# Kernel tuning notes

Measured on AMD Instinct MI355X. Metric: run time of the kernel, lower is better.

## Reference

```python
import jax, jax.numpy as jnp
import numpy as np

B, C, H, W, HEADS = 4, 192, 128, 128, 8
C2 = 2 * C
DN = ('NCHW', 'OIHW', 'NCHW')


def conv1x1(x, w, b):
    o = jax.lax.conv_general_dilated(x, w, (1, 1), 'VALID', dimension_numbers=DN)
    return o + b[None, :, None, None]


def gconv3(x, w, b):
    # grouped 3x3 conv: groups = C, channels = 2C -> 2 in / 2 out channels per group
    o = jax.lax.conv_general_dilated(x, w, (1, 1), 'SAME', dimension_numbers=DN,
                                     feature_group_count=C)
    return o + b[None, :, None, None]


def l2norm(t):
    # torch F.normalize(dim=-1, eps=1e-12)
    n = jnp.linalg.norm(t, axis=-1, keepdims=True)
    return t / jnp.maximum(n, 1e-12)


def setup_inputs() -> dict:
    key = jax.random.key(0)
    ks = jax.random.split(key, 16)
    s = 0.02
    inp = {
        'x': jax.random.normal(ks[0], (B, C, H, W), jnp.float32),
        'y': jax.random.normal(ks[1], (B, C, H, W), jnp.float32),
        'kv_w': jax.random.normal(ks[2], (C2, C, 1, 1), jnp.float32) * s,
        'kv_b': jax.random.normal(ks[3], (C2,), jnp.float32) * s,
        'kv_dw_w': jax.random.normal(ks[4], (C2, 2, 3, 3), jnp.float32) * s,
        'kv_dw_b': jax.random.normal(ks[5], (C2,), jnp.float32) * s,
        'q_w': jax.random.normal(ks[6], (C2, C, 1, 1), jnp.float32) * s,
        'q_b': jax.random.normal(ks[7], (C2,), jnp.float32) * s,
        'q_dw_w': jax.random.normal(ks[8], (C2, 2, 3, 3), jnp.float32) * s,
        'q_dw_b': jax.random.normal(ks[9], (C2,), jnp.float32) * s,
        'ky_w': jax.random.normal(ks[10], (C2, C, 1, 1), jnp.float32) * s,
        'ky_b': jax.random.normal(ks[11], (C2,), jnp.float32) * s,
        'ky_dw_w': jax.random.normal(ks[12], (C2, 2, 3, 3), jnp.float32) * s,
        'ky_dw_b': jax.random.normal(ks[13], (C2,), jnp.float32) * s,
        'temperature': jnp.ones((HEADS, 1, 1), jnp.float32),
        'gamma1': jnp.full((1,), 0.1, jnp.float32),
        'gamma2': jnp.full((1,), 0.1, jnp.float32),
    }
    return inp


def reference(x, y, kv_w, kv_b, kv_dw_w, kv_dw_b, q_w, q_b, q_dw_w, q_dw_b,
              ky_w, ky_b, ky_dw_w, ky_dw_b, temperature, gamma1, gamma2):
    b, c, h, w = x.shape
    ch = c // HEADS  # channels per head

    x_mid = x + y
    q = gconv3(conv1x1(x_mid, kv_w, kv_b), kv_dw_w, kv_dw_b)
    q1, q2 = jnp.split(q, 2, axis=1)
    kvx = gconv3(conv1x1(x, q_w, q_b), q_dw_w, q_dw_b)
    kx, vx = jnp.split(kvx, 2, axis=1)
    kvy = gconv3(conv1x1(y, ky_w, ky_b), ky_dw_w, ky_dw_b)
    ky_, vy = jnp.split(kvy, 2, axis=1)

    def to_heads(t):  # (b, head*ch, h, w) -> (b, head, ch, h*w)
        return t.reshape(b, HEADS, ch, h * w)

    q1, q2, kx, ky_, vx, vy = map(to_heads, (q1, q2, kx, ky_, vx, vy))
    q1, q2, kx, ky_ = map(l2norm, (q1, q2, kx, ky_))

    attn = (jnp.einsum('bhcn,bhdn->bhcd', q1, ky_) +
            jnp.einsum('bhcn,bhdn->bhcd', q2, kx)) * temperature[None]
    attn = jax.nn.softmax(attn, axis=-1)  # (b, head, c, c), tiny c

    out1 = jnp.einsum('bhcd,bhdn->bhcn', attn, vx)
    out2 = jnp.einsum('bhcd,bhdn->bhcn', attn, vy)
    out = gamma1[0] * out1 + gamma2[0] * out2
    return out.reshape(b, c, h, w)
```

## Files before the change

### kernel.cpp

```cpp
#include <hip/hip_runtime.h>
#include <hip/hip_bf16.h>
#include <stdint.h>

#define NUM_B 4
#define NUM_C 192
#define NUM_C2 384
#define NUM_H 128
#define NUM_W 128
#define NUM_N 16384
#define NHEADS 8
#define CHD 24

#define NKC 128
#define PSTRIDE 1280

typedef float f32x4_t __attribute__((ext_vector_type(4)));
typedef float f32x2_t __attribute__((ext_vector_type(2)));
typedef __bf16 bf16x8_t __attribute__((ext_vector_type(8)));
typedef unsigned short u16x8_t __attribute__((ext_vector_type(8)));

__device__ __forceinline__ float bf2f(unsigned short u){
  union { unsigned int i; float f; } v; v.i = ((unsigned int)u) << 16; return v.f;
}
__device__ __forceinline__ unsigned short f2bf(float f){
  union { float f; unsigned int i; } v; v.f = f;
  unsigned int x = v.i;
  x += 0x7fffu + ((x >> 16) & 1u);
  return (unsigned short)(x >> 16);
}
__device__ __forceinline__ unsigned short f2bf_n(float f){
  union { __bf16 h; unsigned short u; } cv; cv.h = (__bf16)f; return cv.u;
}

__global__ __launch_bounds__(256) void prepack_w3(
    const float* __restrict__ W0, const float* __restrict__ W1,
    const float* __restrict__ W2, unsigned short* __restrict__ out)
{
  int tid = blockIdx.x * 256 + threadIdx.x;
  if (tid >= 9216) return;
  const float* W = (blockIdx.y == 0) ? W0 : (blockIdx.y == 1) ? W1 : W2;
  unsigned short* o_ = out + (size_t)blockIdx.y * 73728;
  int c = tid & 3;
  int o = (tid >> 2) & 127;
  int s = (tid >> 9) % 6;
  int ot = tid / 3072;
  int sw = c ^ ((o >> 1) & 3);
  const float* src = W + (size_t)(ot * 128 + o) * NUM_C + s * 32 + sw * 8;
  f32x4_t f0 = *(const f32x4_t*)src;
  f32x4_t f1 = *(const f32x4_t*)(src + 4);
  u16x8_t pk;
  pk[0] = f2bf(f0[0]); pk[1] = f2bf(f0[1]); pk[2] = f2bf(f0[2]); pk[3] = f2bf(f0[3]);
  pk[4] = f2bf(f1[0]); pk[5] = f2bf(f1[1]); pk[6] = f2bf(f1[2]); pk[7] = f2bf(f1[3]);
  *(u16x8_t*)(o_ + (size_t)tid * 8) = pk;
}

__global__ __launch_bounds__(256) void prepack_in(
    const float* __restrict__ x, const float* __restrict__ y,
    unsigned short* __restrict__ xb, unsigned short* __restrict__ yb)
{
  const int t = threadIdx.x;
  const int nt = blockIdx.x, s = blockIdx.y, b = blockIdx.z;
  const float* px = x + (size_t)b * NUM_C * NUM_N + (size_t)s * 32 * NUM_N + nt * 128;
  const float* py = y + (size_t)b * NUM_C * NUM_N + (size_t)s * 32 * NUM_N + nt * 128;
  size_t obase = ((size_t)(b * 128 + nt) * 6 + s) * 4096;
  #pragma unroll
  for (int i = 0; i < 2; i++){
    int u = t + 256 * i;
    int n = u >> 2, slot = u & 3;
    int c = slot ^ ((n >> 1) & 3);
    const float* sx = px + (size_t)(c * 8) * NUM_N + n;
    const float* sy = py + (size_t)(c * 8) * NUM_N + n;
    u16x8_t ox, oy;
    #pragma unroll
    for (int kk = 0; kk < 8; kk++){
      ox[kk] = f2bf_n(sx[(size_t)kk * NUM_N]);
      oy[kk] = f2bf_n(sy[(size_t)kk * NUM_N]);
    }
    *(u16x8_t*)(xb + obase + (size_t)u * 8) = ox;
    *(u16x8_t*)(yb + obase + (size_t)u * 8) = oy;
  }
}

__global__ __launch_bounds__(256, 4) void conv1x1_fused(
    const unsigned short* __restrict__ xb, const unsigned short* __restrict__ yb,
    const unsigned short* __restrict__ Wpk,
    const float* __restrict__ b0, const float* __restrict__ b1,
    const float* __restrict__ b2, unsigned short* __restrict__ z3)
{
  __shared__ __align__(16) unsigned short As[2][4096];
  __shared__ __align__(16) unsigned short Bs[2][4096];
  const int d = blockIdx.x;
  const int xcd = d & 7;
  const int rest = d >> 3;
  const int j = rest % 9;
  const int m_ = (rest / 9) * 8 + xcd;
  const int br = j / 3;
  const int ot = j % 3;
  const int nt = m_ & 127;
  const int b  = m_ >> 7;
  const int t = threadIdx.x;
  const int lane = t & 63;
  const int wv = t >> 6;
  const int wr = wv >> 1, wc = wv & 1;
  const int o0 = ot * 128;
  const int n0 = nt * 128;

  const unsigned short* Bp0 = (br == 2) ? yb : xb;
  const unsigned short* Bp1 = yb;
  const int add2 = (br == 0);
  const unsigned short* Wb = Wpk + (size_t)br * 73728;
  const float* bias = (br == 0) ? b0 : (br == 1) ? b1 : b2;
  unsigned short* zout = z3 + (size_t)br * NUM_B * NUM_C2 * NUM_N;

  f32x4_t acc[4][4];
  const f32x4_t zz = {0.f, 0.f, 0.f, 0.f};
  #pragma unroll
  for (int m = 0; m < 4; m++)
    #pragma unroll
    for (int nf = 0; nf < 4; nf++) acc[m][nf] = zz;

  u16x8_t areg[2], breg[2], breg2[2];

  auto loadA = [&](int ks){
    const u16x8_t* gp = (const u16x8_t*)(Wb + (size_t)(ot * 6 + ks) * 4096);
    areg[0] = gp[t];
    areg[1] = gp[t + 256];
  };
  auto loadB = [&](int ks){
    size_t off = ((size_t)(b * 128 + nt) * 6 + ks) * 4096;
    const u16x8_t* gp = (const u16x8_t*)(Bp0 + off);
    breg[0] = gp[t];
    breg[1] = gp[t + 256];
    if (add2){
      const u16x8_t* gp2 = (const u16x8_t*)(Bp1 + off);
      breg2[0] = gp2[t];
      breg2[1] = gp2[t + 256];
    }
  };
  auto writeA = [&](int buf){
    *(u16x8_t*)(&As[buf][(size_t)t * 8]) = areg[0];
    *(u16x8_t*)(&As[buf][(size_t)(t + 256) * 8]) = areg[1];
  };
  auto writeB = [&](int buf){
    if (!add2){
      *(u16x8_t*)(&Bs[buf][(size_t)t * 8]) = breg[0];
      *(u16x8_t*)(&Bs[buf][(size_t)(t + 256) * 8]) = breg[1];
    } else {
      #pragma unroll
      for (int i = 0; i < 2; i++){
        u16x8_t r;
        #pragma unroll
        for (int jj = 0; jj < 8; jj++)
          r[jj] = f2bf_n(bf2f(breg[i][jj]) + bf2f(breg2[i][jj]));
        *(u16x8_t*)(&Bs[buf][(size_t)(t + 256 * i) * 8]) = r;
      }
    }
  };

  auto compute = [&](int buf){
    const int rsel = lane & 15;
    const int g = lane >> 4;
    bf16x8_t af[4], bfr[4];
    #pragma unroll
    for (int m = 0; m < 4; m++){
      int r = wr * 64 + m * 16 + rsel;
      int sw = g ^ ((r >> 1) & 3);
      af[m] = *(const bf16x8_t*)(&As[buf][r * 32 + sw * 8]);
    }
    #pragma unroll
    for (int nf = 0; nf < 4; nf++){
      int r = wc * 64 + nf * 16 + rsel;
      int sw = g ^ ((r >> 1) & 3);
      bfr[nf] = *(const bf16x8_t*)(&Bs[buf][r * 32 + sw * 8]);
    }
    #pragma unroll
    for (int m = 0; m < 4; m++)
      #pragma unroll
      for (int nf = 0; nf < 4; nf++)
        acc[m][nf] = __builtin_amdgcn_mfma_f32_16x16x32_bf16(af[m], bfr[nf], acc[m][nf], 0, 0, 0);
  };

  loadA(0); loadB(0);
  writeA(0); writeB(0);
  __syncthreads();
  int buf = 0;
  #pragma unroll 1
  for (int ks = 0; ks < 6; ks++){
    if (ks < 5){
      loadA(ks + 1);
      loadB(ks + 1);
    }
    compute(buf);
    if (ks < 5){
      writeA(buf ^ 1);
      writeB(buf ^ 1);
      __syncthreads();
    }
    buf ^= 1;
  }

  const int colb = lane & 15;
  const int rsub = (lane >> 4) * 4;
  #pragma unroll
  for (int m = 0; m < 4; m++){
    #pragma unroll
    for (int nf = 0; nf < 4; nf++){
      int col = n0 + wc * 64 + nf * 16 + colb;
      #pragma unroll
      for (int r = 0; r < 4; r++){
        int o = o0 + wr * 64 + m * 16 + rsub + r;
        float v = acc[m][nf][r] + bias[o];
        zout[((size_t)b * NUM_C2 + o) * NUM_N + col] = f2bf_n(v);
      }
    }
  }
}

__global__ __launch_bounds__(256) void gconv3_dw(
    const unsigned short* __restrict__ z,
    const float* __restrict__ dww, const float* __restrict__ dwb,
    unsigned short* __restrict__ outq)
{
  const int t = threadIdx.x;
  const int wo = t & 15;
  const int hh = t >> 4;
  const int h = blockIdx.x * 16 + hh;
  const int g = blockIdx.y;
  const int b = blockIdx.z;

  float v[2][3][8];
  #pragma unroll
  for (int ic = 0; ic < 2; ic++){
    const unsigned short* src = z + ((size_t)b * NUM_C2 + 2 * g + ic) * NUM_N;
    #pragma unroll
    for (int dy = 0; dy < 3; dy++){
      int row = h + dy - 1;
      if (row >= 0 && row < NUM_H){
        u16x8_t raw = *(const u16x8_t*)(src + row * NUM_W + wo * 8);
        #pragma unroll
        for (int jj = 0; jj < 8; jj++) v[ic][dy][jj] = bf2f(raw[jj]);
      } else {
        #pragma unroll
        for (int jj = 0; jj < 8; jj++) v[ic][dy][jj] = 0.f;
      }
    }
  }
  float lft[2][3], rgt[2][3];
  #pragma unroll
  for (int ic = 0; ic < 2; ic++)
    #pragma unroll
    for (int dy = 0; dy < 3; dy++){
      float l = __shfl_up(v[ic][dy][7], 1u, 64);
      float r = __shfl_down(v[ic][dy][0], 1u, 64);
      lft[ic][dy] = (wo == 0)  ? 0.f : l;
      rgt[ic][dy] = (wo == 15) ? 0.f : r;
    }
  #pragma unroll
  for (int oc2 = 0; oc2 < 2; oc2++){
    const int oc = 2 * g + oc2;
    float wgt[2][9];
    #pragma unroll
    for (int ic = 0; ic < 2; ic++)
      #pragma unroll
      for (int k9 = 0; k9 < 9; k9++)
        wgt[ic][k9] = dww[(size_t)oc * 18 + ic * 9 + k9];
    float bia = dwb[oc];
    u16x8_t st;
    #pragma unroll
    for (int w8 = 0; w8 < 8; w8++){
      float s = bia;
      #pragma unroll
      for (int ic = 0; ic < 2; ic++)
        #pragma unroll
        for (int ky = 0; ky < 3; ky++)
          #pragma unroll
          for (int kx = 0; kx < 3; kx++){
            int wx = w8 + kx - 1;
            float xv = (wx < 0) ? lft[ic][ky] : ((wx > 7) ? rgt[ic][ky] : v[ic][ky][wx]);
            s += wgt[ic][ky * 3 + kx] * xv;
          }
      st[w8] = f2bf(s);
    }
    *(u16x8_t*)(outq + ((size_t)b * NUM_C2 + oc) * NUM_N + h * NUM_W + wo * 8) = st;
  }
}

__global__ __launch_bounds__(64) void dots_kernel(
    const unsigned short* __restrict__ qkv0, const unsigned short* __restrict__ qkv1,
    const unsigned short* __restrict__ qkv2, float* __restrict__ dpart)
{
  const int lane = threadIdx.x;
  const int kc = blockIdx.x;
  const int h = blockIdx.y;
  const int b = blockIdx.z;
  const unsigned short* q1 = qkv0 + ((size_t)b * NUM_C2 + h * CHD) * NUM_N;
  const unsigned short* q2 = qkv0 + ((size_t)b * NUM_C2 + NUM_C + h * CHD) * NUM_N;
  const unsigned short* kx = qkv1 + ((size_t)b * NUM_C2 + h * CHD) * NUM_N;
  const unsigned short* ky = qkv2 + ((size_t)b * NUM_C2 + h * CHD) * NUM_N;

  const f32x4_t zz = {0.f, 0.f, 0.f, 0.f};
  f32x4_t d1[2][2], d2[2][2], nrm[4][2];
  #pragma unroll
  for (int i = 0; i < 2; i++)
    #pragma unroll
    for (int j = 0; j < 2; j++){ d1[i][j] = zz; d2[i][j] = zz; }
  #pragma unroll
  for (int tn = 0; tn < 4; tn++){ nrm[tn][0] = zz; nrm[tn][1] = zz; }

  const int row = lane & 15;
  const int kl = (lane >> 4) * 8;
  const int r0 = row;
  const int r1 = (16 + row < CHD) ? (16 + row) : (CHD - 1);
  #pragma unroll
  for (int ks = 0; ks < 4; ks++){
    const size_t k0 = (size_t)kc * 128 + ks * 32 + kl;
    const size_t off0 = (size_t)r0 * NUM_N + k0;
    const size_t off1 = (size_t)r1 * NUM_N + k0;
    bf16x8_t fq1[2], fq2[2], fkx[2], fky[2];
    fq1[0] = *(const bf16x8_t*)(q1 + off0);  fq1[1] = *(const bf16x8_t*)(q1 + off1);
    fq2[0] = *(const bf16x8_t*)(q2 + off0);  fq2[1] = *(const bf16x8_t*)(q2 + off1);
    fkx[0] = *(const bf16x8_t*)(kx + off0);  fkx[1] = *(const bf16x8_t*)(kx + off1);
    fky[0] = *(const bf16x8_t*)(ky + off0);  fky[1] = *(const bf16x8_t*)(ky + off1);
    #pragma unroll
    for (int i = 0; i < 2; i++)
      #pragma unroll
      for (int j = 0; j < 2; j++){
        d1[i][j] = __builtin_amdgcn_mfma_f32_16x16x32_bf16(fq1[i], fky[j], d1[i][j], 0, 0, 0);
        d2[i][j] = __builtin_amdgcn_mfma_f32_16x16x32_bf16(fq2[i], fkx[j], d2[i][j], 0, 0, 0);
      }
    #pragma unroll
    for (int rg = 0; rg < 2; rg++){
      nrm[0][rg] = __builtin_amdgcn_mfma_f32_16x16x32_bf16(fq1[rg], fq1[rg], nrm[0][rg], 0, 0, 0);
      nrm[1][rg] = __builtin_amdgcn_mfma_f32_16x16x32_bf16(fq2[rg], fq2[rg], nrm[1][rg], 0, 0, 0);
      nrm[2][rg] = __builtin_amdgcn_mfma_f32_16x16x32_bf16(fkx[rg], fkx[rg], nrm[2][rg], 0, 0, 0);
      nrm[3][rg] = __builtin_amdgcn_mfma_f32_16x16x32_bf16(fky[rg], fky[rg], nrm[3][rg], 0, 0, 0);
    }
  }

  float* P = dpart + ((size_t)kc * (NUM_B * NHEADS) + (b * NHEADS + h)) * PSTRIDE;
  const int colb = lane & 15;
  const int rb = (lane >> 4) * 4;
  #pragma unroll
  for (int i = 0; i < 2; i++)
    #pragma unroll
    for (int j = 0; j < 2; j++){
      int cc = j * 16 + colb;
      if (cc < CHD){
        #pragma unroll
        for (int r = 0; r < 4; r++){
          int rr = i * 16 + rb + r;
          if (rr < CHD){
            P[rr * CHD + cc] = d1[i][j][r];
            P[576 + rr * CHD + cc] = d2[i][j][r];
          }
        }
      }
    }
  #pragma unroll
  for (int tn = 0; tn < 4; tn++)
    #pragma unroll
    for (int rg = 0; rg < 2; rg++){
      int cc = rg * 16 + colb;
      #pragma unroll
      for (int r = 0; r < 4; r++){
        int rr = rg * 16 + rb + r;
        if (rr == cc && rr < CHD) P[1152 + tn * CHD + rr] = nrm[tn][rg][r];
      }
    }
}

__global__ __launch_bounds__(256) void reduce_dots(
    const float* __restrict__ dpart,
    float* __restrict__ dots1, float* __restrict__ dots2, float* __restrict__ norms)
{
  const int slot = blockIdx.x * 256 + threadIdx.x;
  const int bh = blockIdx.y;
  if (slot >= 1248) return;
  float s = 0.f;
  #pragma unroll 4
  for (int kc = 0; kc < NKC; kc++)
    s += dpart[((size_t)kc * (NUM_B * NHEADS) + bh) * PSTRIDE + slot];
  if (slot < 576)        dots1[(size_t)bh * 576 + slot] = s;
  else if (slot < 1152)  dots2[(size_t)bh * 576 + (slot - 576)] = s;
  else                   norms[(size_t)bh * 96 + (slot - 1152)] = s;
}

__global__ __launch_bounds__(64) void softmax_kernel(
    const float* __restrict__ dots1, const float* __restrict__ dots2,
    const float* __restrict__ norms, const float* __restrict__ temp,
    float* __restrict__ attn)
{
  const int c = threadIdx.x;
  const int bh = blockIdx.x;
  if (c >= CHD) return;
  const int h = bh & 7;
  const float* D1 = dots1 + (size_t)bh * CHD * CHD;
  const float* D2 = dots2 + (size_t)bh * CHD * CHD;
  const float* NB = norms + (size_t)bh * 4 * CHD;
  float n1 = fmaxf(sqrtf(NB[0 * CHD + c]), 1e-12f);
  float n2 = fmaxf(sqrtf(NB[1 * CHD + c]), 1e-12f);
  float T = temp[h];
  float l[CHD];
  float m = -1e30f;
  #pragma unroll
  for (int d = 0; d < CHD; d++){
    float nx = fmaxf(sqrtf(NB[2 * CHD + d]), 1e-12f);
    float ny = fmaxf(sqrtf(NB[3 * CHD + d]), 1e-12f);
    float e = (D1[c * CHD + d] / (n1 * ny) + D2[c * CHD + d] / (n2 * nx)) * T;
    l[d] = e; m = fmaxf(m, e);
  }
  float s = 0.f;
  #pragma unroll
  for (int d = 0; d < CHD; d++){ float p = expf(l[d] - m); l[d] = p; s += p; }
  float inv = 1.f / s;
  float* A = attn + (size_t)bh * CHD * CHD + c * CHD;
  #pragma unroll
  for (int d = 0; d < CHD; d++) A[d] = l[d] * inv;
}

__global__ __launch_bounds__(256) void out_kernel(
    const unsigned short* __restrict__ qkv1, const unsigned short* __restrict__ qkv2,
    const float* __restrict__ attn,
    const float* __restrict__ g1, const float* __restrict__ g2,
    float* __restrict__ out)
{
  __shared__ float A[CHD * CHD];
  const int t = threadIdx.x;
  const int nc = blockIdx.x, hq = blockIdx.y, b = blockIdx.z;
  const float* Ag = attn + (size_t)(b * NHEADS + hq) * CHD * CHD;
  for (int i = t; i < CHD * CHD; i += 256) A[i] = Ag[i];
  __syncthreads();
  const int n = nc * 512 + t * 2;
  const unsigned short* vx = qkv1 + ((size_t)b * NUM_C2 + NUM_C + hq * CHD) * NUM_N + n;
  const unsigned short* vy = qkv2 + ((size_t)b * NUM_C2 + NUM_C + hq * CHD) * NUM_N + n;
  float vxa[CHD], vxb[CHD], vya[CHD], vyb[CHD];
  #pragma unroll
  for (int d = 0; d < CHD; d++){
    unsigned int rx = *(const unsigned int*)(vx + (size_t)d * NUM_N);
    unsigned int ry = *(const unsigned int*)(vy + (size_t)d * NUM_N);
    vxa[d] = bf2f((unsigned short)(rx & 0xffffu));
    vxb[d] = bf2f((unsigned short)(rx >> 16));
    vya[d] = bf2f((unsigned short)(ry & 0xffffu));
    vyb[d] = bf2f((unsigned short)(ry >> 16));
  }
  const float G1 = g1[0], G2 = g2[0];
  float* ob = out + ((size_t)b * NUM_C + hq * CHD) * NUM_N + n;
  #pragma unroll
  for (int cq = 0; cq < CHD; cq++){
    float ax = 0.f, bx = 0.f, ay = 0.f, by = 0.f;
    #pragma unroll
    for (int d = 0; d < CHD; d++){
      float a = A[cq * CHD + d];
      ax += a * vxa[d]; bx += a * vxb[d];
      ay += a * vya[d]; by += a * vyb[d];
    }
    f32x2_t st = {G1 * ax + G2 * ay, G1 * bx + G2 * by};
    *(f32x2_t*)(ob + (size_t)cq * NUM_N) = st;
  }
}

extern "C" void kernel_launch(void* const* d_in, const int* in_sizes, int n_in,
                              void* d_out, int out_size, void* d_ws, size_t ws_size,
                              hipStream_t stream)
{
  const float* x = (const float*)d_in[0];
  const float* y = (const float*)d_in[1];
  const float* conv_b[3] = {(const float*)d_in[3], (const float*)d_in[7], (const float*)d_in[11]};
  const float* dw_w[3]   = {(const float*)d_in[4], (const float*)d_in[8], (const float*)d_in[12]};
  const float* dw_b[3]   = {(const float*)d_in[5], (const float*)d_in[9], (const float*)d_in[13]};
  const float* conv_w[3] = {(const float*)d_in[2], (const float*)d_in[6], (const float*)d_in[10]};
  const float* temp = (const float*)d_in[14];
  const float* g1 = (const float*)d_in[15];
  const float* g2 = (const float*)d_in[16];
  float* out = (float*)d_out;

  char* ws = (char*)d_ws;
  const size_t ZB = (size_t)NUM_B * NUM_C2 * NUM_N * 2;
  unsigned short* xb   = (unsigned short*)ws;
  unsigned short* yb   = (unsigned short*)(ws + 25165824);
  unsigned short* z3   = (unsigned short*)(ws + 50331648);
  unsigned short* qkv0 = (unsigned short*)ws;
  unsigned short* qkv1 = (unsigned short*)(ws + 50331648);
  unsigned short* qkv2 = (unsigned short*)(ws + 100663296);
  float* dpart         = (float*)(ws + 150994944);
  float* dots1 = (float*)(ws + 201326592);
  float* dots2 = dots1 + NUM_B * NHEADS * CHD * CHD;
  float* norms = dots2 + NUM_B * NHEADS * CHD * CHD;
  float* attn  = norms + NUM_B * NHEADS * 4 * CHD;
  unsigned short* Wpk = (unsigned short*)(attn + NUM_B * NHEADS * CHD * CHD);

  prepack_w3<<<dim3(36, 3), 256, 0, stream>>>(conv_w[0], conv_w[1], conv_w[2], Wpk);
  prepack_in<<<dim3(128, 6, NUM_B), 256, 0, stream>>>(x, y, xb, yb);

  conv1x1_fused<<<4608, 256, 0, stream>>>(xb, yb, Wpk,
                                          conv_b[0], conv_b[1], conv_b[2], z3);

  dim3 gd(NUM_H / 16, NUM_C, NUM_B), bd(256);
  unsigned short* zb0 = z3;
  unsigned short* zb1 = z3 + ZB / 2;
  unsigned short* zb2 = z3 + ZB;
  gconv3_dw<<<gd, bd, 0, stream>>>(zb0, dw_w[0], dw_b[0], qkv0);
  gconv3_dw<<<gd, bd, 0, stream>>>(zb1, dw_w[1], dw_b[1], qkv1);
  gconv3_dw<<<gd, bd, 0, stream>>>(zb2, dw_w[2], dw_b[2], qkv2);

  dots_kernel<<<dim3(NKC, NHEADS, NUM_B), 64, 0, stream>>>(qkv0, qkv1, qkv2, dpart);
  reduce_dots<<<dim3(5, NUM_B * NHEADS), 256, 0, stream>>>(dpart, dots1, dots2, norms);
  softmax_kernel<<<dim3(NUM_B * NHEADS), 64, 0, stream>>>(dots1, dots2, norms, temp, attn);
  out_kernel<<<dim3(32, NHEADS, NUM_B), 256, 0, stream>>>(qkv1, qkv2, attn, g1, g2, out);
}
```

Before: 238.5 us.

## Store conv1x1 output channel-interleaved by four and fuse reduce with softmax

The 1x1 conv epilogue now writes bf16 output in a layout that interleaves four channels per pixel, so each lane issues one 8-byte vector store instead of four scalar 2-byte stores. The depthwise kernel is rewritten to read that layout, handling four channels (two groups) per block with 64-byte contiguous loads. The dot-product reduction and softmax kernels are merged into one launch, which removes an intermediate global round trip. The risk is that the reduction now runs on only 32 blocks, leaving it less parallel.

```diff
diff --git a/kernel.cpp b/kernel.cpp
--- a/kernel.cpp
+++ b/kernel.cpp
@@ -18,6 +18,7 @@
 typedef float f32x2_t __attribute__((ext_vector_type(2)));
 typedef __bf16 bf16x8_t __attribute__((ext_vector_type(8)));
 typedef unsigned short u16x8_t __attribute__((ext_vector_type(8)));
+typedef unsigned short u16x4_t __attribute__((ext_vector_type(4)));
 
 __device__ __forceinline__ float bf2f(unsigned short u){
   union { unsigned int i; float f; } v; v.i = ((unsigned int)u) << 16; return v.f;
@@ -102,7 +103,6 @@
   const int lane = t & 63;
   const int wv = t >> 6;
   const int wr = wv >> 1, wc = wv & 1;
-  const int o0 = ot * 128;
   const int n0 = nt * 128;
 
   const unsigned short* Bp0 = (br == 2) ? yb : xb;
@@ -200,24 +200,24 @@
   }
 
   const int colb = lane & 15;
-  const int rsub = (lane >> 4) * 4;
+  const int ob_l = lane >> 4;
   #pragma unroll
   for (int m = 0; m < 4; m++){
+    int o_blk = ot * 32 + wr * 16 + m * 4 + ob_l;
     #pragma unroll
     for (int nf = 0; nf < 4; nf++){
       int col = n0 + wc * 64 + nf * 16 + colb;
-      #pragma unroll
-      for (int r = 0; r < 4; r++){
-        int o = o0 + wr * 64 + m * 16 + rsub + r;
-        float v = acc[m][nf][r] + bias[o];
-        zout[((size_t)b * NUM_C2 + o) * NUM_N + col] = f2bf_n(v);
-      }
-    }
-  }
-}
-
-__global__ __launch_bounds__(256) void gconv3_dw(
-    const unsigned short* __restrict__ z,
+      u16x4_t pk;
+      #pragma unroll
+      for (int r = 0; r < 4; r++)
+        pk[r] = f2bf_n(acc[m][nf][r] + bias[o_blk * 4 + r]);
+      *(u16x4_t*)(zout + (((size_t)b * 96 + o_blk) * NUM_N + col) * 4) = pk;
+    }
+  }
+}
+
+__global__ __launch_bounds__(256) void gconv4_dw(
+    const unsigned short* __restrict__ zp,
     const float* __restrict__ dww, const float* __restrict__ dwb,
     unsigned short* __restrict__ outq)
 {
@@ -225,60 +225,70 @@
   const int wo = t & 15;
   const int hh = t >> 4;
   const int h = blockIdx.x * 16 + hh;
-  const int g = blockIdx.y;
+  const int g2 = blockIdx.y;
   const int b = blockIdx.z;
 
-  float v[2][3][8];
-  #pragma unroll
-  for (int ic = 0; ic < 2; ic++){
-    const unsigned short* src = z + ((size_t)b * NUM_C2 + 2 * g + ic) * NUM_N;
+  float v[4][3][8];
+  const unsigned short* src = zp + (size_t)(b * 96 + g2) * NUM_N * 4;
+  #pragma unroll
+  for (int dy = 0; dy < 3; dy++){
+    int row = h + dy - 1;
+    if (row >= 0 && row < NUM_H){
+      const unsigned short* base = src + (size_t)(row * NUM_W + wo * 8) * 4;
+      u16x8_t ch[4];
+      #pragma unroll
+      for (int q = 0; q < 4; q++) ch[q] = *(const u16x8_t*)(base + q * 8);
+      #pragma unroll
+      for (int jw = 0; jw < 8; jw++)
+        #pragma unroll
+        for (int c = 0; c < 4; c++){
+          int idx = jw * 4 + c;
+          v[c][dy][jw] = bf2f(ch[idx >> 3][idx & 7]);
+        }
+    } else {
+      #pragma unroll
+      for (int c = 0; c < 4; c++)
+        #pragma unroll
+        for (int jw = 0; jw < 8; jw++) v[c][dy][jw] = 0.f;
+    }
+  }
+  float lft[4][3], rgt[4][3];
+  #pragma unroll
+  for (int c = 0; c < 4; c++)
     #pragma unroll
     for (int dy = 0; dy < 3; dy++){
-      int row = h + dy - 1;
-      if (row >= 0 && row < NUM_H){
-        u16x8_t raw = *(const u16x8_t*)(src + row * NUM_W + wo * 8);
-        #pragma unroll
-        for (int jj = 0; jj < 8; jj++) v[ic][dy][jj] = bf2f(raw[jj]);
-      } else {
-        #pragma unroll
-        for (int jj = 0; jj < 8; jj++) v[ic][dy][jj] = 0.f;
-      }
-    }
-  }
-  float lft[2][3], rgt[2][3];
-  #pragma unroll
-  for (int ic = 0; ic < 2; ic++)
-    #pragma unroll
-    for (int dy = 0; dy < 3; dy++){
-      float l = __shfl_up(v[ic][dy][7], 1u, 64);
-      float r = __shfl_down(v[ic][dy][0], 1u, 64);
-      lft[ic][dy] = (wo == 0)  ? 0.f : l;
-      rgt[ic][dy] = (wo == 15) ? 0.f : r;
-    }
-  #pragma unroll
-  for (int oc2 = 0; oc2 < 2; oc2++){
-    const int oc = 2 * g + oc2;
+      float l = __shfl_up(v[c][dy][7], 1u, 64);
+      float r = __shfl_down(v[c][dy][0], 1u, 64);
+      lft[c][dy] = (wo == 0)  ? 0.f : l;
+      rgt[c][dy] = (wo == 15) ? 0.f : r;
+    }
+  #pragma unroll
+  for (int c = 0; c < 4; c++){
+    const int oc = g2 * 4 + c;
+    const int ci0 = c & 2;
     float wgt[2][9];
     #pragma unroll
-    for (int ic = 0; ic < 2; ic++)
+    for (int icg = 0; icg < 2; icg++)
       #pragma unroll
       for (int k9 = 0; k9 < 9; k9++)
-        wgt[ic][k9] = dww[(size_t)oc * 18 + ic * 9 + k9];
+        wgt[icg][k9] = dww[(size_t)oc * 18 + icg * 9 + k9];
     float bia = dwb[oc];
     u16x8_t st;
     #pragma unroll
     for (int w8 = 0; w8 < 8; w8++){
       float s = bia;
       #pragma unroll
-      for (int ic = 0; ic < 2; ic++)
+      for (int icg = 0; icg < 2; icg++){
+        const int ci = ci0 + icg;
         #pragma unroll
         for (int ky = 0; ky < 3; ky++)
           #pragma unroll
           for (int kx = 0; kx < 3; kx++){
             int wx = w8 + kx - 1;
-            float xv = (wx < 0) ? lft[ic][ky] : ((wx > 7) ? rgt[ic][ky] : v[ic][ky][wx]);
-            s += wgt[ic][ky * 3 + kx] * xv;
+            float xv = (wx < 0) ? lft[ci][ky] : ((wx > 7) ? rgt[ci][ky] : v[ci][ky][wx]);
+            s += wgt[icg][ky * 3 + kx] * xv;
           }
+      }
       st[w8] = f2bf(s);
     }
     *(u16x8_t*)(outq + ((size_t)b * NUM_C2 + oc) * NUM_N + h * NUM_W + wo * 8) = st;
@@ -369,53 +379,46 @@
     }
 }
 
-__global__ __launch_bounds__(256) void reduce_dots(
-    const float* __restrict__ dpart,
-    float* __restrict__ dots1, float* __restrict__ dots2, float* __restrict__ norms)
-{
-  const int slot = blockIdx.x * 256 + threadIdx.x;
-  const int bh = blockIdx.y;
-  if (slot >= 1248) return;
-  float s = 0.f;
-  #pragma unroll 4
-  for (int kc = 0; kc < NKC; kc++)
-    s += dpart[((size_t)kc * (NUM_B * NHEADS) + bh) * PSTRIDE + slot];
-  if (slot < 576)        dots1[(size_t)bh * 576 + slot] = s;
-  else if (slot < 1152)  dots2[(size_t)bh * 576 + (slot - 576)] = s;
-  else                   norms[(size_t)bh * 96 + (slot - 1152)] = s;
-}
-
-__global__ __launch_bounds__(64) void softmax_kernel(
-    const float* __restrict__ dots1, const float* __restrict__ dots2,
-    const float* __restrict__ norms, const float* __restrict__ temp,
+__global__ __launch_bounds__(256) void reduce_softmax(
+    const float* __restrict__ dpart, const float* __restrict__ temp,
     float* __restrict__ attn)
 {
-  const int c = threadIdx.x;
+  __shared__ float D1[576], D2[576], NB[96];
   const int bh = blockIdx.x;
-  if (c >= CHD) return;
-  const int h = bh & 7;
-  const float* D1 = dots1 + (size_t)bh * CHD * CHD;
-  const float* D2 = dots2 + (size_t)bh * CHD * CHD;
-  const float* NB = norms + (size_t)bh * 4 * CHD;
-  float n1 = fmaxf(sqrtf(NB[0 * CHD + c]), 1e-12f);
-  float n2 = fmaxf(sqrtf(NB[1 * CHD + c]), 1e-12f);
-  float T = temp[h];
-  float l[CHD];
-  float m = -1e30f;
-  #pragma unroll
-  for (int d = 0; d < CHD; d++){
-    float nx = fmaxf(sqrtf(NB[2 * CHD + d]), 1e-12f);
-    float ny = fmaxf(sqrtf(NB[3 * CHD + d]), 1e-12f);
-    float e = (D1[c * CHD + d] / (n1 * ny) + D2[c * CHD + d] / (n2 * nx)) * T;
-    l[d] = e; m = fmaxf(m, e);
-  }
-  float s = 0.f;
-  #pragma unroll
-  for (int d = 0; d < CHD; d++){ float p = expf(l[d] - m); l[d] = p; s += p; }
-  float inv = 1.f / s;
-  float* A = attn + (size_t)bh * CHD * CHD + c * CHD;
-  #pragma unroll
-  for (int d = 0; d < CHD; d++) A[d] = l[d] * inv;
+  const int t = threadIdx.x;
+  for (int slot = t; slot < 1248; slot += 256){
+    float s = 0.f;
+    #pragma unroll 4
+    for (int kc = 0; kc < NKC; kc++)
+      s += dpart[((size_t)kc * (NUM_B * NHEADS) + bh) * PSTRIDE + slot];
+    if (slot < 576)        D1[slot] = s;
+    else if (slot < 1152)  D2[slot - 576] = s;
+    else                   NB[slot - 1152] = s;
+  }
+  __syncthreads();
+  if (t < CHD){
+    const int c = t;
+    const int h = bh & 7;
+    float n1 = fmaxf(sqrtf(NB[0 * CHD + c]), 1e-12f);
+    float n2 = fmaxf(sqrtf(NB[1 * CHD + c]), 1e-12f);
+    float T = temp[h];
+    float l[CHD];
+    float m = -1e30f;
+    #pragma unroll
+    for (int d = 0; d < CHD; d++){
+      float nx = fmaxf(sqrtf(NB[2 * CHD + d]), 1e-12f);
+      float ny = fmaxf(sqrtf(NB[3 * CHD + d]), 1e-12f);
+      float e = (D1[c * CHD + d] / (n1 * ny) + D2[c * CHD + d] / (n2 * nx)) * T;
+      l[d] = e; m = fmaxf(m, e);
+    }
+    float s = 0.f;
+    #pragma unroll
+    for (int d = 0; d < CHD; d++){ float p = expf(l[d] - m); l[d] = p; s += p; }
+    float inv = 1.f / s;
+    float* A = attn + (size_t)bh * CHD * CHD + c * CHD;
+    #pragma unroll
+    for (int d = 0; d < CHD; d++) A[d] = l[d] * inv;
+  }
 }
 
 __global__ __launch_bounds__(256) void out_kernel(
@@ -483,10 +486,7 @@
   unsigned short* qkv1 = (unsigned short*)(ws + 50331648);
   unsigned short* qkv2 = (unsigned short*)(ws + 100663296);
   float* dpart         = (float*)(ws + 150994944);
-  float* dots1 = (float*)(ws + 201326592);
-  float* dots2 = dots1 + NUM_B * NHEADS * CHD * CHD;
-  float* norms = dots2 + NUM_B * NHEADS * CHD * CHD;
-  float* attn  = norms + NUM_B * NHEADS * 4 * CHD;
+  float* attn  = (float*)(ws + 201326592);
   unsigned short* Wpk = (unsigned short*)(attn + NUM_B * NHEADS * CHD * CHD);
 
   prepack_w3<<<dim3(36, 3), 256, 0, stream>>>(conv_w[0], conv_w[1], conv_w[2], Wpk);
@@ -495,16 +495,15 @@
   conv1x1_fused<<<4608, 256, 0, stream>>>(xb, yb, Wpk,
                                           conv_b[0], conv_b[1], conv_b[2], z3);
 
-  dim3 gd(NUM_H / 16, NUM_C, NUM_B), bd(256);
+  dim3 gd(NUM_H / 16, 96, NUM_B), bd(256);
   unsigned short* zb0 = z3;
   unsigned short* zb1 = z3 + ZB / 2;
   unsigned short* zb2 = z3 + ZB;
-  gconv3_dw<<<gd, bd, 0, stream>>>(zb0, dw_w[0], dw_b[0], qkv0);
-  gconv3_dw<<<gd, bd, 0, stream>>>(zb1, dw_w[1], dw_b[1], qkv1);
-  gconv3_dw<<<gd, bd, 0, stream>>>(zb2, dw_w[2], dw_b[2], qkv2);
+  gconv4_dw<<<gd, bd, 0, stream>>>(zb0, dw_w[0], dw_b[0], qkv0);
+  gconv4_dw<<<gd, bd, 0, stream>>>(zb1, dw_w[1], dw_b[1], qkv1);
+  gconv4_dw<<<gd, bd, 0, stream>>>(zb2, dw_w[2], dw_b[2], qkv2);
 
   dots_kernel<<<dim3(NKC, NHEADS, NUM_B), 64, 0, stream>>>(qkv0, qkv1, qkv2, dpart);
-  reduce_dots<<<dim3(5, NUM_B * NHEADS), 256, 0, stream>>>(dpart, dots1, dots2, norms);
-  softmax_kernel<<<dim3(NUM_B * NHEADS), 64, 0, stream>>>(dots1, dots2, norms, temp, attn);
+  reduce_softmax<<<dim3(NUM_B * NHEADS), 256, 0, stream>>>(dpart, temp, attn);
   out_kernel<<<dim3(32, NHEADS, NUM_B), 256, 0, stream>>>(qkv1, qkv2, attn, g1, g2, out);
 }
```

After: 278.3 us. +16.7%, slower.
